# Performance work log

Measured on AMD Instinct MI355X. Metric: run time of the kernel, lower is better.

Reference implementation:

```python
import jax, jax.numpy as jnp
import numpy as np

B, T, V, LSRC, D = 4, 128, 50257, 512, 512
PAD_ID = 0
GAMMA1, GAMMA2 = 1.0, 0.1
BETA, MAX_ITER = 2.0, 400


def setup_inputs() -> dict:
    key = jax.random.key(0)
    ks = jax.random.split(key, 7)
    # output_mle are per-token probabilities (original takes torch.log of them)
    output_mle = jax.random.uniform(ks[0], (B, T, V), jnp.float32, 1e-4, 1.0)
    attn_dist = jax.random.uniform(ks[1], (B, LSRC, T), jnp.float32)
    coverage = jax.random.uniform(ks[2], (B, LSRC, T), jnp.float32)
    trg = jax.random.randint(ks[3], (B, T), 0, V)
    dec_mask = jax.random.randint(ks[4], (B, T), 0, 2).astype(bool)
    dec_len = jax.random.randint(ks[5], (B,), 1, T)
    W_emb = jax.random.normal(ks[6], (V, D), jnp.float32) * 0.02
    return {"output_mle": output_mle, "attn_dist": attn_dist, "coverage": coverage,
            "trg": trg, "dec_mask": dec_mask, "dec_len": dec_len, "W_emb": W_emb}


def ipot(a1, a2, beta=BETA, max_iter=MAX_ITER):
    # a1, a2: [n, d_hid] (already flattened from [B, T, d_hid])
    n = a1.shape[0]
    a1n = a1 / jnp.linalg.norm(a1, axis=1, keepdims=True)
    a2n = a2 / jnp.linalg.norm(a2, axis=1, keepdims=True)
    C = a1n @ a2n.T                      # [n, n] cosine cost
    A = jnp.exp(-C / beta)
    eye = jnp.eye(n, dtype=C.dtype)
    sigma0 = jnp.full((n, 1), 1.0 / n, C.dtype)
    T0 = jnp.full((n, n), 1.0 / (n * n), C.dtype)

    def step(carry, _):
        Tm, sigma = carry
        Q = A * Tm
        dvec = 1.0 / n / (Q @ sigma)          # [n, 1]
        sigma = 1.0 / n / (Q.T @ dvec)        # [n, 1]
        # Faithful to torch source: diag(d) * Q * diag(sigma) is ELEMENTWISE,
        # so only the diagonal of the product survives.
        Tm = dvec * Q * sigma.T * eye
        return (Tm, sigma), None

    (Tm, _), _ = jax.lax.scan(step, (T0, sigma0), None, length=max_iter)
    return jnp.sum(Tm * C)


def reference(output_mle, attn_dist, coverage, trg, dec_mask, dec_len, W_emb):
    # --- NLL loss (Eq. 6): mean -log p[target] over non-pad tokens ---
    logp = jnp.log(output_mle)
    tok_lp = jnp.take_along_axis(logp, trg[..., None], axis=-1)[..., 0]   # [B, T]
    valid = (trg != PAD_ID)
    nll = -jnp.sum(jnp.where(valid, tok_lp, 0.0)) / jnp.sum(valid).astype(logp.dtype)

    # --- Coverage loss (Eq. 12) ---
    cov = jnp.sum(jnp.minimum(attn_dist, coverage), axis=1)               # [B, T]
    cov = jnp.where(dec_mask, 0.0, cov)
    cov_loss = jnp.sum(cov) / jnp.sum(dec_len).astype(cov.dtype)

    # --- OT loss via IPOT ---
    trg_emb = W_emb[trg]                                                  # [B, T, D]
    probs = jax.nn.softmax(output_mle, axis=-1)
    pred = jnp.einsum('btv,vd->btd', probs, W_emb)                        # [B, T, D]
    ot = ipot(pred.reshape(-1, D), trg_emb.reshape(-1, D))

    # Faithful to source: gamma2 added as a constant (not multiplied by ot)
    return nll + GAMMA1 * cov_loss + GAMMA2 + ot
```

## Files before the change

### kernel.cpp

```cpp
#include <hip/hip_runtime.h>
#include <math.h>

#define B_ 4
#define T_ 128
#define V_ 50257
#define D_ 512
#define NROWS 512
#define GAMMA2_ 0.1f

#define BK 32
#define KC 1600
#define SPLITK 32
#define NIT (KC / BK)
#define LDA 40
#define LDB 40

#define SLICE (NROWS * D_)

typedef __attribute__((ext_vector_type(8))) short s8v;
typedef __attribute__((ext_vector_type(4))) float f4v;

#define WS_PART_OFF 1024

__device__ inline unsigned int pack2bf(float f0, float f1) {
    unsigned int u0 = __float_as_uint(f0);
    unsigned int u1 = __float_as_uint(f1);
    u0 += 0x7fffu + ((u0 >> 16) & 1u);
    u1 += 0x7fffu + ((u1 >> 16) & 1u);
    return (u0 >> 16) | (u1 & 0xffff0000u);
}

__device__ inline void sync_lds() {
    __builtin_amdgcn_s_waitcnt(0xC07F);
    __builtin_amdgcn_s_barrier();
}

__device__ inline float wave_reduce(float v) {
    #pragma unroll
    for (int o = 32; o > 0; o >>= 1) v += __shfl_down(v, o, 64);
    return v;
}

__global__ void misc_kernel(const float* __restrict__ output_mle,
                            const float* __restrict__ attn,
                            const float* __restrict__ cover,
                            const int* __restrict__ trg,
                            const int* __restrict__ dec_mask,
                            const int* __restrict__ dec_len,
                            float* __restrict__ acc) {
    int bid = blockIdx.x;
    if (bid < 64) {
        float s = 0.f;
        const float4* a4 = (const float4*)attn;
        const float4* c4 = (const float4*)cover;
        for (int i4 = bid * 256 + threadIdx.x; i4 < 65536; i4 += 64 * 256) {
            float4 a = a4[i4];
            float4 c = c4[i4];
            int b = i4 >> 14;
            int t = (i4 << 2) & (T_ - 1);
            int4 m = *(const int4*)&dec_mask[(b << 7) + t];
            s += m.x ? 0.f : fminf(a.x, c.x);
            s += m.y ? 0.f : fminf(a.y, c.y);
            s += m.z ? 0.f : fminf(a.z, c.z);
            s += m.w ? 0.f : fminf(a.w, c.w);
        }
        s = wave_reduce(s);
        if ((threadIdx.x & 63) == 0) atomicAdd(&acc[2], s);
    } else {
        float lp = 0.f, cnt = 0.f;
        for (int i = threadIdx.x; i < NROWS; i += 256) {
            int tg = trg[i];
            if (tg != 0) {
                lp += __logf(output_mle[(size_t)i * V_ + tg]);
                cnt += 1.f;
            }
        }
        lp = wave_reduce(lp); cnt = wave_reduce(cnt);
        if ((threadIdx.x & 63) == 0) { atomicAdd(&acc[0], lp); atomicAdd(&acc[1], cnt); }
        if (threadIdx.x < B_) atomicAdd(&acc[3], (float)dec_len[threadIdx.x]);
    }
}

__launch_bounds__(256)
__global__ void gemm_kernel(const float* __restrict__ X,
                            const float* __restrict__ W,
                            float* __restrict__ part,
                            int use_atomic) {
    __shared__ __align__(16) short As[128 * LDA];
    __shared__ __align__(16) short Bs[128 * LDB];

    const int bx   = blockIdx.x;
    const int xcd  = bx & 7;
    const int j    = bx >> 3;
    const int s    = xcd + 8 * (j >> 4);
    const int tile = j & 15;
    const int i0   = (tile & 3) * 128;
    const int d0   = (tile >> 2) * 128;
    const int ks   = s * KC;
    const int ke   = min(ks + KC, V_);

    const int tid  = threadIdx.x;
    const int lane = tid & 63;
    const int wave = tid >> 6;
    const int wm   = (wave & 1) * 64;
    const int wn   = (wave >> 1) * 64;
    const int l15  = lane & 15;
    const int l4   = lane >> 4;

    const int ar   = tid >> 1;
    const int akh  = (tid & 1) * 16;
    const int bn2  = (tid & 63) * 2;
    const int bkq  = (tid >> 6) * 8;

    f4v acc[4][4];
    #pragma unroll
    for (int a = 0; a < 4; a++)
        #pragma unroll
        for (int b = 0; b < 4; b++) acc[a][b] = (f4v)0.f;

    auto stageA = [&](const float4 (&ab)[4]) {
        const float* f = (const float*)&ab[0];
        unsigned int au[8];
        #pragma unroll
        for (int p = 0; p < 8; p++)
            au[p] = pack2bf(__expf(f[2 * p]), __expf(f[2 * p + 1]));
        *(uint4*)&As[ar * LDA + akh]     = *(const uint4*)&au[0];
        *(uint4*)&As[ar * LDA + akh + 8] = *(const uint4*)&au[4];
    };
    auto stageB = [&](const float2 (&bb)[8]) {
        unsigned int r0[4], r1[4];
        #pragma unroll
        for (int p = 0; p < 4; p++) {
            r0[p] = pack2bf(bb[2 * p].x, bb[2 * p + 1].x);
            r1[p] = pack2bf(bb[2 * p].y, bb[2 * p + 1].y);
        }
        *(uint4*)&Bs[bn2 * LDB + bkq]       = *(const uint4*)&r0[0];
        *(uint4*)&Bs[(bn2 + 1) * LDB + bkq] = *(const uint4*)&r1[0];
    };
    auto domfma = [&]() {
        s8v af[4], bfr[4];
        #pragma unroll
        for (int mi = 0; mi < 4; mi++)
            af[mi] = *(const s8v*)&As[(wm + mi * 16 + l15) * LDA + l4 * 8];
        #pragma unroll
        for (int ni = 0; ni < 4; ni++)
            bfr[ni] = *(const s8v*)&Bs[(wn + ni * 16 + l15) * LDB + l4 * 8];
        #pragma unroll
        for (int mi = 0; mi < 4; mi++)
            #pragma unroll
            for (int ni = 0; ni < 4; ni++)
                acc[mi][ni] = __builtin_amdgcn_mfma_f32_16x16x32_bf16(
                    af[mi], bfr[ni], acc[mi][ni], 0, 0, 0);
    };
    auto issue = [&](float4 (&ab)[4], float2 (&bb)[8], const float* ap, const float* bp) {
        #pragma unroll
        for (int q = 0; q < 4; q++) ab[q] = *(const float4*)(ap + q * 4);
        #pragma unroll
        for (int j2 = 0; j2 < 8; j2++) bb[j2] = *(const float2*)(bp + (size_t)j2 * D_);
    };

    if (ks + KC <= V_) {
        const float* ap = X + (size_t)(i0 + ar) * V_ + ks + akh;
        const float* bp = W + d0 + bn2 + (size_t)(ks + bkq) * D_;
        float4 a0[4], a1[4];
        float2 b0[8], b1[8];
        issue(a0, b0, ap, bp);
        #pragma unroll 1
        for (int it = 0; it < NIT; it += 2) {
            ap += BK; bp += (size_t)BK * D_;
            if (it + 1 < NIT) issue(a1, b1, ap, bp);
            sync_lds();
            stageA(a0); stageB(b0);
            sync_lds();
            domfma();

            ap += BK; bp += (size_t)BK * D_;
            if (it + 2 < NIT) issue(a0, b0, ap, bp);
            sync_lds();
            stageA(a1); stageB(b1);
            sync_lds();
            domfma();
        }
    } else {
        const float* Abase = X + (size_t)(i0 + ar) * V_;
        const float* Bbase = W + d0 + bn2;
        for (int k0 = ks; k0 < ke; k0 += BK) {
            float4 ab[4];
            float2 bb[8];
            #pragma unroll
            for (int q = 0; q < 4; q++) {
                int gk = min(k0 + akh + q * 4, V_ - 4);
                ab[q] = *(const float4*)(Abase + gk);
            }
            #pragma unroll
            for (int j2 = 0; j2 < 8; j2++) {
                int gk = min(k0 + bkq + j2, V_ - 1);
                bb[j2] = *(const float2*)(Bbase + (size_t)gk * D_);
            }
            sync_lds();
            {
                unsigned int au[8];
                const float* f = (const float*)&ab[0];
                #pragma unroll
                for (int p = 0; p < 8; p++) {
                    int g0 = k0 + akh + 2 * p;
                    float e0 = (g0     < ke) ? __expf(f[2 * p])     : 0.f;
                    float e1 = (g0 + 1 < ke) ? __expf(f[2 * p + 1]) : 0.f;
                    au[p] = pack2bf(e0, e1);
                }
                *(uint4*)&As[ar * LDA + akh]     = *(const uint4*)&au[0];
                *(uint4*)&As[ar * LDA + akh + 8] = *(const uint4*)&au[4];
            }
            {
                unsigned int r0[4], r1[4];
                #pragma unroll
                for (int p = 0; p < 4; p++) {
                    int g0 = k0 + bkq + 2 * p;
                    float x0 = (g0     < ke) ? bb[2 * p].x     : 0.f;
                    float x1 = (g0 + 1 < ke) ? bb[2 * p + 1].x : 0.f;
                    float y0 = (g0     < ke) ? bb[2 * p].y     : 0.f;
                    float y1 = (g0 + 1 < ke) ? bb[2 * p + 1].y : 0.f;
                    r0[p] = pack2bf(x0, x1);
                    r1[p] = pack2bf(y0, y1);
                }
                *(uint4*)&Bs[bn2 * LDB + bkq]       = *(const uint4*)&r0[0];
                *(uint4*)&Bs[(bn2 + 1) * LDB + bkq] = *(const uint4*)&r1[0];
            }
            sync_lds();
            domfma();
        }
    }

    float* dst = part + (use_atomic ? 0 : (size_t)s * SLICE);
    #pragma unroll
    for (int mi = 0; mi < 4; mi++) {
        #pragma unroll
        for (int ni = 0; ni < 4; ni++) {
            int col = d0 + wn + ni * 16 + l15;
            #pragma unroll
            for (int r = 0; r < 4; r++) {
                int row = i0 + wm + mi * 16 + l4 * 4 + r;
                if (use_atomic) atomicAdd(&dst[row * D_ + col], acc[mi][ni][r]);
                else            dst[row * D_ + col] = acc[mi][ni][r];
            }
        }
    }
}

__global__ void ot_kernel(const float* __restrict__ part,
                          const float* __restrict__ W,
                          const int* __restrict__ trg,
                          float* __restrict__ acc,
                          int nsl) {
    __shared__ float Ps[4][D_];
    int wave = threadIdx.x >> 6, lane = threadIdx.x & 63;
    int row  = blockIdx.x;
    const size_t off = (size_t)row * D_ + lane * 8;

    float4 p0 = {0, 0, 0, 0}, p1 = {0, 0, 0, 0};
    for (int s = wave; s < nsl; s += 4) {
        const float4* ps = (const float4*)(part + (size_t)s * SLICE + off);
        float4 q0 = ps[0], q1 = ps[1];
        p0.x += q0.x; p0.y += q0.y; p0.z += q0.z; p0.w += q0.w;
        p1.x += q1.x; p1.y += q1.y; p1.z += q1.z; p1.w += q1.w;
    }
    *(float4*)&Ps[wave][lane * 8]     = p0;
    *(float4*)&Ps[wave][lane * 8 + 4] = p1;
    __syncthreads();
    if (wave == 0) {
        float4 s0 = {0, 0, 0, 0}, s1 = {0, 0, 0, 0};
        #pragma unroll
        for (int w = 0; w < 4; w++) {
            float4 q0 = *(const float4*)&Ps[w][lane * 8];
            float4 q1 = *(const float4*)&Ps[w][lane * 8 + 4];
            s0.x += q0.x; s0.y += q0.y; s0.z += q0.z; s0.w += q0.w;
            s1.x += q1.x; s1.y += q1.y; s1.z += q1.z; s1.w += q1.w;
        }
        const float4* t4 = (const float4*)(W + (size_t)trg[row] * D_ + lane * 8);
        float4 t0 = t4[0], t1 = t4[1];

        float dot = s0.x * t0.x + s0.y * t0.y + s0.z * t0.z + s0.w * t0.w
                  + s1.x * t1.x + s1.y * t1.y + s1.z * t1.z + s1.w * t1.w;
        float nn  = s0.x * s0.x + s0.y * s0.y + s0.z * s0.z + s0.w * s0.w
                  + s1.x * s1.x + s1.y * s1.y + s1.z * s1.z + s1.w * s1.w;
        float tt  = t0.x * t0.x + t0.y * t0.y + t0.z * t0.z + t0.w * t0.w
                  + t1.x * t1.x + t1.y * t1.y + t1.z * t1.z + t1.w * t1.w;

        dot = wave_reduce(dot); nn = wave_reduce(nn); tt = wave_reduce(tt);
        if (lane == 0)
            atomicAdd(&acc[4], (dot / sqrtf(nn * tt)) * (1.0f / (float)NROWS));
    }
}

__global__ void finalize_kernel(const float* __restrict__ acc, float* __restrict__ out) {
    if (threadIdx.x == 0)
        out[0] = -acc[0] / acc[1] + acc[2] / acc[3] + GAMMA2_ + acc[4];
}

extern "C" void kernel_launch(void* const* d_in, const int* in_sizes, int n_in,
                              void* d_out, int out_size, void* d_ws, size_t ws_size,
                              hipStream_t stream) {
    const float* output_mle = (const float*)d_in[0];
    const float* attn       = (const float*)d_in[1];
    const float* cover      = (const float*)d_in[2];
    const int*   trg        = (const int*)d_in[3];
    const int*   dec_mask   = (const int*)d_in[4];
    const int*   dec_len    = (const int*)d_in[5];
    const float* W          = (const float*)d_in[6];
    float* out  = (float*)d_out;
    float* acc  = (float*)d_ws;
    float* part = acc + WS_PART_OFF;

    const size_t need = (size_t)WS_PART_OFF * 4 + (size_t)SPLITK * SLICE * 4;
    const bool partial = (ws_size >= need);

    if (partial) {
        hipMemsetAsync(d_ws, 0, WS_PART_OFF * sizeof(float), stream);
    } else {
        hipMemsetAsync(d_ws, 0, (WS_PART_OFF + SLICE) * sizeof(float), stream);
    }
    misc_kernel<<<65, 256, 0, stream>>>(output_mle, attn, cover, trg, dec_mask, dec_len, acc);
    gemm_kernel<<<16 * SPLITK, 256, 0, stream>>>(output_mle, W, part, partial ? 0 : 1);
    ot_kernel<<<NROWS, 256, 0, stream>>>(part, W, trg, acc, partial ? SPLITK : 1);
    finalize_kernel<<<1, 64, 0, stream>>>(acc, out);
}
```

Before: 315.5 us.

## Fuse misc kernel into GEMM launch and widen GEMM blocks to 512 threads

The misc reductions (coverage and NLL) now run as extra leading blocks of the GEMM launch, which removes one kernel launch. The GEMM block grows from 256 to 512 threads, using 8 waves each with a 64x32 sub-tile instead of 4 waves with 64x64, so each thread stages less data and holds fewer accumulators. The ot_kernel is templated on the slice count so its reduction loop can be unrolled. The trade-off is less MFMA work per wave relative to the LDS fragment loads, and a launch-bounds hint that limits registers per thread.

```diff
diff --git a/kernel.cpp b/kernel.cpp
--- a/kernel.cpp
+++ b/kernel.cpp
@@ -14,6 +14,7 @@
 #define NIT (KC / BK)
 #define LDA 40
 #define LDB 40
+#define NMISC 40
 
 #define SLICE (NROWS * D_)
 
@@ -41,19 +42,21 @@
     return v;
 }
 
-__global__ void misc_kernel(const float* __restrict__ output_mle,
-                            const float* __restrict__ attn,
-                            const float* __restrict__ cover,
-                            const int* __restrict__ trg,
-                            const int* __restrict__ dec_mask,
-                            const int* __restrict__ dec_len,
-                            float* __restrict__ acc) {
-    int bid = blockIdx.x;
-    if (bid < 64) {
+__device__ void misc_body512(int bid,
+                             const float* __restrict__ output_mle,
+                             const float* __restrict__ attn,
+                             const float* __restrict__ cover,
+                             const int* __restrict__ trg,
+                             const int* __restrict__ dec_mask,
+                             const int* __restrict__ dec_len,
+                             float* __restrict__ acc) {
+    const int tid = threadIdx.x;
+    if (bid < 32) {
         float s = 0.f;
         const float4* a4 = (const float4*)attn;
         const float4* c4 = (const float4*)cover;
-        for (int i4 = bid * 256 + threadIdx.x; i4 < 65536; i4 += 64 * 256) {
+        #pragma unroll 1
+        for (int i4 = bid * 512 + tid; i4 < 65536; i4 += 32 * 512) {
             float4 a = a4[i4];
             float4 c = c4[i4];
             int b = i4 >> 14;
@@ -65,33 +68,43 @@
             s += m.w ? 0.f : fminf(a.w, c.w);
         }
         s = wave_reduce(s);
-        if ((threadIdx.x & 63) == 0) atomicAdd(&acc[2], s);
-    } else {
+        if ((tid & 63) == 0) atomicAdd(&acc[2], s);
+    } else if (bid == 32) {
         float lp = 0.f, cnt = 0.f;
-        for (int i = threadIdx.x; i < NROWS; i += 256) {
-            int tg = trg[i];
+        if (tid < NROWS) {
+            int tg = trg[tid];
             if (tg != 0) {
-                lp += __logf(output_mle[(size_t)i * V_ + tg]);
-                cnt += 1.f;
+                lp = __logf(output_mle[(size_t)tid * V_ + tg]);
+                cnt = 1.f;
             }
         }
         lp = wave_reduce(lp); cnt = wave_reduce(cnt);
-        if ((threadIdx.x & 63) == 0) { atomicAdd(&acc[0], lp); atomicAdd(&acc[1], cnt); }
-        if (threadIdx.x < B_) atomicAdd(&acc[3], (float)dec_len[threadIdx.x]);
-    }
-}
-
-__launch_bounds__(256)
+        if ((tid & 63) == 0) { atomicAdd(&acc[0], lp); atomicAdd(&acc[1], cnt); }
+        if (tid < B_) atomicAdd(&acc[3], (float)dec_len[tid]);
+    }
+}
+
+__launch_bounds__(512, 4)
 __global__ void gemm_kernel(const float* __restrict__ X,
                             const float* __restrict__ W,
+                            const float* __restrict__ attn,
+                            const float* __restrict__ cover,
+                            const int* __restrict__ trg,
+                            const int* __restrict__ dec_mask,
+                            const int* __restrict__ dec_len,
+                            float* __restrict__ acc,
                             float* __restrict__ part,
                             int use_atomic) {
     __shared__ __align__(16) short As[128 * LDA];
     __shared__ __align__(16) short Bs[128 * LDB];
 
-    const int bx   = blockIdx.x;
-    const int xcd  = bx & 7;
-    const int j    = bx >> 3;
+    if (blockIdx.x < NMISC) {
+        misc_body512(blockIdx.x, X, attn, cover, trg, dec_mask, dec_len, acc);
+        return;
+    }
+    const int g    = blockIdx.x - NMISC;
+    const int xcd  = g & 7;
+    const int j    = g >> 3;
     const int s    = xcd + 8 * (j >> 4);
     const int tile = j & 15;
     const int i0   = (tile & 3) * 128;
@@ -102,68 +115,64 @@
     const int tid  = threadIdx.x;
     const int lane = tid & 63;
     const int wave = tid >> 6;
-    const int wm   = (wave & 1) * 64;
-    const int wn   = (wave >> 1) * 64;
+    const int wm   = (wave >> 2) * 64;
+    const int wn   = (wave & 3) * 32;
     const int l15  = lane & 15;
     const int l4   = lane >> 4;
 
-    const int ar   = tid >> 1;
-    const int akh  = (tid & 1) * 16;
+    const int ar   = tid >> 2;
+    const int ak   = (tid & 3) * 8;
     const int bn2  = (tid & 63) * 2;
-    const int bkq  = (tid >> 6) * 8;
-
-    f4v acc[4][4];
+    const int bk   = (tid >> 6) * 4;
+
+    f4v acc_[4][2];
     #pragma unroll
     for (int a = 0; a < 4; a++)
         #pragma unroll
-        for (int b = 0; b < 4; b++) acc[a][b] = (f4v)0.f;
-
-    auto stageA = [&](const float4 (&ab)[4]) {
+        for (int b = 0; b < 2; b++) acc_[a][b] = (f4v)0.f;
+
+    auto stageA = [&](const float4 (&ab)[2]) {
         const float* f = (const float*)&ab[0];
-        unsigned int au[8];
-        #pragma unroll
-        for (int p = 0; p < 8; p++)
+        unsigned int au[4];
+        #pragma unroll
+        for (int p = 0; p < 4; p++)
             au[p] = pack2bf(__expf(f[2 * p]), __expf(f[2 * p + 1]));
-        *(uint4*)&As[ar * LDA + akh]     = *(const uint4*)&au[0];
-        *(uint4*)&As[ar * LDA + akh + 8] = *(const uint4*)&au[4];
+        *(uint4*)&As[ar * LDA + ak] = *(const uint4*)&au[0];
     };
-    auto stageB = [&](const float2 (&bb)[8]) {
-        unsigned int r0[4], r1[4];
-        #pragma unroll
-        for (int p = 0; p < 4; p++) {
-            r0[p] = pack2bf(bb[2 * p].x, bb[2 * p + 1].x);
-            r1[p] = pack2bf(bb[2 * p].y, bb[2 * p + 1].y);
-        }
-        *(uint4*)&Bs[bn2 * LDB + bkq]       = *(const uint4*)&r0[0];
-        *(uint4*)&Bs[(bn2 + 1) * LDB + bkq] = *(const uint4*)&r1[0];
+    auto stageB = [&](const float2 (&bb)[4]) {
+        unsigned int r0[2], r1[2];
+        r0[0] = pack2bf(bb[0].x, bb[1].x); r0[1] = pack2bf(bb[2].x, bb[3].x);
+        r1[0] = pack2bf(bb[0].y, bb[1].y); r1[1] = pack2bf(bb[2].y, bb[3].y);
+        *(uint2*)&Bs[bn2 * LDB + bk]       = *(const uint2*)&r0[0];
+        *(uint2*)&Bs[(bn2 + 1) * LDB + bk] = *(const uint2*)&r1[0];
     };
     auto domfma = [&]() {
-        s8v af[4], bfr[4];
+        s8v af[4], bfr[2];
         #pragma unroll
         for (int mi = 0; mi < 4; mi++)
             af[mi] = *(const s8v*)&As[(wm + mi * 16 + l15) * LDA + l4 * 8];
         #pragma unroll
-        for (int ni = 0; ni < 4; ni++)
+        for (int ni = 0; ni < 2; ni++)
             bfr[ni] = *(const s8v*)&Bs[(wn + ni * 16 + l15) * LDB + l4 * 8];
         #pragma unroll
         for (int mi = 0; mi < 4; mi++)
             #pragma unroll
-            for (int ni = 0; ni < 4; ni++)
-                acc[mi][ni] = __builtin_amdgcn_mfma_f32_16x16x32_bf16(
-                    af[mi], bfr[ni], acc[mi][ni], 0, 0, 0);
+            for (int ni = 0; ni < 2; ni++)
+                acc_[mi][ni] = __builtin_amdgcn_mfma_f32_16x16x32_bf16(
+                    af[mi], bfr[ni], acc_[mi][ni], 0, 0, 0);
     };
-    auto issue = [&](float4 (&ab)[4], float2 (&bb)[8], const float* ap, const float* bp) {
-        #pragma unroll
-        for (int q = 0; q < 4; q++) ab[q] = *(const float4*)(ap + q * 4);
-        #pragma unroll
-        for (int j2 = 0; j2 < 8; j2++) bb[j2] = *(const float2*)(bp + (size_t)j2 * D_);
+    auto issue = [&](float4 (&ab)[2], float2 (&bb)[4], const float* ap, const float* bp) {
+        ab[0] = *(const float4*)(ap);
+        ab[1] = *(const float4*)(ap + 4);
+        #pragma unroll
+        for (int j2 = 0; j2 < 4; j2++) bb[j2] = *(const float2*)(bp + (size_t)j2 * D_);
     };
 
     if (ks + KC <= V_) {
-        const float* ap = X + (size_t)(i0 + ar) * V_ + ks + akh;
-        const float* bp = W + d0 + bn2 + (size_t)(ks + bkq) * D_;
-        float4 a0[4], a1[4];
-        float2 b0[8], b1[8];
+        const float* ap = X + (size_t)(i0 + ar) * V_ + ks + ak;
+        const float* bp = W + d0 + bn2 + (size_t)(ks + bk) * D_;
+        float4 a0[2], a1[2];
+        float2 b0[4], b1[4];
         issue(a0, b0, ap, bp);
         #pragma unroll 1
         for (int it = 0; it < NIT; it += 2) {
@@ -185,46 +194,44 @@
         const float* Abase = X + (size_t)(i0 + ar) * V_;
         const float* Bbase = W + d0 + bn2;
         for (int k0 = ks; k0 < ke; k0 += BK) {
-            float4 ab[4];
-            float2 bb[8];
+            float4 ab[2];
+            float2 bb[4];
             #pragma unroll
-            for (int q = 0; q < 4; q++) {
-                int gk = min(k0 + akh + q * 4, V_ - 4);
+            for (int q = 0; q < 2; q++) {
+                int gk = min(k0 + ak + q * 4, V_ - 4);
                 ab[q] = *(const float4*)(Abase + gk);
             }
             #pragma unroll
-            for (int j2 = 0; j2 < 8; j2++) {
-                int gk = min(k0 + bkq + j2, V_ - 1);
+            for (int j2 = 0; j2 < 4; j2++) {
+                int gk = min(k0 + bk + j2, V_ - 1);
                 bb[j2] = *(const float2*)(Bbase + (size_t)gk * D_);
             }
             sync_lds();
             {
-                unsigned int au[8];
+                unsigned int au[4];
                 const float* f = (const float*)&ab[0];
                 #pragma unroll
-                for (int p = 0; p < 8; p++) {
-                    int g0 = k0 + akh + 2 * p;
+                for (int p = 0; p < 4; p++) {
+                    int g0 = k0 + ak + 2 * p;
                     float e0 = (g0     < ke) ? __expf(f[2 * p])     : 0.f;
                     float e1 = (g0 + 1 < ke) ? __expf(f[2 * p + 1]) : 0.f;
                     au[p] = pack2bf(e0, e1);
                 }
-                *(uint4*)&As[ar * LDA + akh]     = *(const uint4*)&au[0];
-                *(uint4*)&As[ar * LDA + akh + 8] = *(const uint4*)&au[4];
+                *(uint4*)&As[ar * LDA + ak] = *(const uint4*)&au[0];
             }
             {
-                unsigned int r0[4], r1[4];
+                float xv[4], yv[4];
                 #pragma unroll
-                for (int p = 0; p < 4; p++) {
-                    int g0 = k0 + bkq + 2 * p;
-                    float x0 = (g0     < ke) ? bb[2 * p].x     : 0.f;
-                    float x1 = (g0 + 1 < ke) ? bb[2 * p + 1].x : 0.f;
-                    float y0 = (g0     < ke) ? bb[2 * p].y     : 0.f;
-                    float y1 = (g0 + 1 < ke) ? bb[2 * p + 1].y : 0.f;
-                    r0[p] = pack2bf(x0, x1);
-                    r1[p] = pack2bf(y0, y1);
+                for (int j2 = 0; j2 < 4; j2++) {
+                    bool ok = (k0 + bk + j2) < ke;
+                    xv[j2] = ok ? bb[j2].x : 0.f;
+                    yv[j2] = ok ? bb[j2].y : 0.f;
                 }
-                *(uint4*)&Bs[bn2 * LDB + bkq]       = *(const uint4*)&r0[0];
-                *(uint4*)&Bs[(bn2 + 1) * LDB + bkq] = *(const uint4*)&r1[0];
+                unsigned int r0[2], r1[2];
+                r0[0] = pack2bf(xv[0], xv[1]); r0[1] = pack2bf(xv[2], xv[3]);
+                r1[0] = pack2bf(yv[0], yv[1]); r1[1] = pack2bf(yv[2], yv[3]);
+                *(uint2*)&Bs[bn2 * LDB + bk]       = *(const uint2*)&r0[0];
+                *(uint2*)&Bs[(bn2 + 1) * LDB + bk] = *(const uint2*)&r1[0];
             }
             sync_lds();
             domfma();
@@ -235,34 +242,38 @@
     #pragma unroll
     for (int mi = 0; mi < 4; mi++) {
         #pragma unroll
-        for (int ni = 0; ni < 4; ni++) {
+        for (int ni = 0; ni < 2; ni++) {
             int col = d0 + wn + ni * 16 + l15;
             #pragma unroll
             for (int r = 0; r < 4; r++) {
                 int row = i0 + wm + mi * 16 + l4 * 4 + r;
-                if (use_atomic) atomicAdd(&dst[row * D_ + col], acc[mi][ni][r]);
-                else            dst[row * D_ + col] = acc[mi][ni][r];
-            }
-        }
-    }
-}
-
+                if (use_atomic) atomicAdd(&dst[row * D_ + col], acc_[mi][ni][r]);
+                else            dst[row * D_ + col] = acc_[mi][ni][r];
+            }
+        }
+    }
+}
+
+template<int NSL>
 __global__ void ot_kernel(const float* __restrict__ part,
                           const float* __restrict__ W,
                           const int* __restrict__ trg,
-                          float* __restrict__ acc,
-                          int nsl) {
+                          float* __restrict__ acc) {
     __shared__ float Ps[4][D_];
     int wave = threadIdx.x >> 6, lane = threadIdx.x & 63;
     int row  = blockIdx.x;
     const size_t off = (size_t)row * D_ + lane * 8;
 
     float4 p0 = {0, 0, 0, 0}, p1 = {0, 0, 0, 0};
-    for (int s = wave; s < nsl; s += 4) {
-        const float4* ps = (const float4*)(part + (size_t)s * SLICE + off);
-        float4 q0 = ps[0], q1 = ps[1];
-        p0.x += q0.x; p0.y += q0.y; p0.z += q0.z; p0.w += q0.w;
-        p1.x += q1.x; p1.y += q1.y; p1.z += q1.z; p1.w += q1.w;
+    #pragma unroll
+    for (int si = 0; si < (NSL + 3) / 4; si++) {
+        int s = wave + 4 * si;
+        if (s < NSL) {
+            const float4* ps = (const float4*)(part + (size_t)s * SLICE + off);
+            float4 q0 = ps[0], q1 = ps[1];
+            p0.x += q0.x; p0.y += q0.y; p0.z += q0.z; p0.w += q0.w;
+            p1.x += q1.x; p1.y += q1.y; p1.z += q1.z; p1.w += q1.w;
+        }
     }
     *(float4*)&Ps[wave][lane * 8]     = p0;
     *(float4*)&Ps[wave][lane * 8 + 4] = p1;
@@ -319,8 +330,9 @@
     } else {
         hipMemsetAsync(d_ws, 0, (WS_PART_OFF + SLICE) * sizeof(float), stream);
     }
-    misc_kernel<<<65, 256, 0, stream>>>(output_mle, attn, cover, trg, dec_mask, dec_len, acc);
-    gemm_kernel<<<16 * SPLITK, 256, 0, stream>>>(output_mle, W, part, partial ? 0 : 1);
-    ot_kernel<<<NROWS, 256, 0, stream>>>(part, W, trg, acc, partial ? SPLITK : 1);
+    gemm_kernel<<<NMISC + 16 * SPLITK, 512, 0, stream>>>(
+        output_mle, W, attn, cover, trg, dec_mask, dec_len, acc, part, partial ? 0 : 1);
+    if (partial) ot_kernel<SPLITK><<<NROWS, 256, 0, stream>>>(part, W, trg, acc);
+    else         ot_kernel<1><<<NROWS, 256, 0, stream>>>(part, W, trg, acc);
     finalize_kernel<<<1, 64, 0, stream>>>(acc, out);
 }
```

Result: faster. 302.1 us (-4.2%).
